# Optimization experiments

Hardware: AMD Instinct MI355X
Metric: run time of the kernel (lower is better)

The kernel has to match this reference:

```python
import jax, jax.numpy as jnp
import numpy as np

N_NODES = 4096
EDGE_PROB = 0.01


def setup_inputs() -> dict:
    key = jax.random.key(0)
    kx, ka, kw = jax.random.split(key, 3)
    x = jax.random.normal(kx, (4, 32, N_NODES, 12), dtype=jnp.float32)
    u = jax.random.uniform(ka, (N_NODES, N_NODES), dtype=jnp.float32)
    adj = (u < EDGE_PROB).astype(jnp.float32)
    adj = jnp.maximum(adj, adj.T)
    weight = jax.random.normal(kw, (3, 32, 32), dtype=jnp.float32) * 0.1
    bias = jnp.zeros((32,), dtype=jnp.float32)
    return {"x": x, "adj": adj, "weight": weight, "bias": bias}


def reference(x, adj, weight, bias):
    # x: [B, c_in, N, T] -> [B, T, N, c_in] as in AdaptiveGraphConv.forward
    B, C, N, T = x.shape
    h = jnp.transpose(x, (0, 3, 2, 1))  # [B, T, N, C]
    # DenseChebConv (K=3): L = I - D^{-1/2} A D^{-1/2}, inf -> 0 for isolated nodes
    d = adj.sum(axis=-1)
    d_inv_sqrt = jnp.where(d > 0, jnp.where(d > 0, d, 1.0) ** -0.5, 0.0)
    norm_adj = d_inv_sqrt[:, None] * adj * d_inv_sqrt[None, :]
    L = jnp.eye(N, dtype=x.dtype) - norm_adj
    Tx0 = h
    Tx1 = jnp.einsum('mn,btnc->btmc', L, h)
    Tx2 = 2.0 * jnp.einsum('mn,btnc->btmc', L, Tx1) - Tx0
    out = (jnp.einsum('btnc,co->btno', Tx0, weight[0])
           + jnp.einsum('btnc,co->btno', Tx1, weight[1])
           + jnp.einsum('btnc,co->btno', Tx2, weight[2])
           + bias)
    # back to [B, c_out, N, T]
    return jnp.transpose(out, (0, 3, 2, 1))
```

## Files before the change

### kernel.cpp

```cpp
#include <hip/hip_runtime.h>

#define NN 4096
#define CC 32
#define TT 12
#define BB 4
#define BT 48
#define NC 1536
#define MAXD 192
#define FW 256
#define NCH 6
#define STP 36
#define SOP 33

typedef float f32x4 __attribute__((ext_vector_type(4)));
typedef short short8 __attribute__((ext_vector_type(8)));

__device__ __forceinline__ float bf2f(unsigned short h) {
  return __uint_as_float(((unsigned int)h) << 16);
}
__device__ __forceinline__ unsigned short f2bf(float f) {
  unsigned int u = __float_as_uint(f);
  return (unsigned short)((u + 0x7FFFu + ((u >> 16) & 1u)) >> 16);
}
__device__ __forceinline__ float blo(unsigned int w) { return __uint_as_float(w << 16); }
__device__ __forceinline__ float bhi(unsigned int w) { return __uint_as_float(w & 0xFFFF0000u); }

__global__ __launch_bounds__(256) void k_build(const float* __restrict__ adj,
                                               uint2* __restrict__ edges,
                                               int* __restrict__ deg, float* __restrict__ dis) {
  __shared__ int cnt;
  int m = blockIdx.x;
  if (threadIdx.x == 0) cnt = 0;
  __syncthreads();
  unsigned int* ecol = (unsigned int*)(edges + m * MAXD);
  const uint4* row = (const uint4*)(adj + (size_t)m * NN);
  for (int i = threadIdx.x; i < NN / 4; i += 256) {
    uint4 v = row[i];
    unsigned int ws[4] = {v.x, v.y, v.z, v.w};
    #pragma unroll
    for (int k = 0; k < 4; ++k) {
      if (ws[k] != 0) {
        int p = atomicAdd(&cnt, 1);
        if (p < MAXD) ecol[p * 2] = (unsigned int)(i * 4 + k);
      }
    }
  }
  __syncthreads();
  if (threadIdx.x == 0) {
    int d = cnt < MAXD ? cnt : MAXD;
    deg[m] = d;
    dis[m] = d > 0 ? (float)(1.0 / sqrt((double)d)) : 0.0f;
  }
}

__global__ __launch_bounds__(192) void k_wt(uint2* __restrict__ edges,
                                            const int* __restrict__ deg,
                                            int* __restrict__ degp,
                                            const float* __restrict__ dis) {
  int m = blockIdx.x;
  int j = threadIdx.x;
  int d = deg[m];
  int dp = (d + 15) & ~15;
  if (j < d) {
    unsigned int* e = (unsigned int*)(edges + m * MAXD + j);
    e[1] = __float_as_uint(dis[e[0]]);
  } else if (j < dp) {
    edges[m * MAXD + j] = make_uint2((unsigned int)m, 0u);
  }
  if (j == 0) degp[m] = dp;
}

__global__ __launch_bounds__(256) void k_trans(const float* __restrict__ x,
                                               unsigned short* __restrict__ H) {
  __shared__ unsigned short sT[192 * STP];
  int b = blockIdx.x >> 8;
  int n0 = (blockIdx.x & 255) * 16;
  int c = threadIdx.x >> 3;
  int l8 = threadIdx.x & 7;
  size_t base = ((size_t)(b * CC + c) * NN + n0) * TT;
  #pragma unroll
  for (int it = 0; it < 6; ++it) {
    int j0 = it * 32 + l8 * 4;
    float4 f = *(const float4*)(x + base + j0);
    sT[(j0 + 0) * STP + c] = f2bf(f.x);
    sT[(j0 + 1) * STP + c] = f2bf(f.y);
    sT[(j0 + 2) * STP + c] = f2bf(f.z);
    sT[(j0 + 3) * STP + c] = f2bf(f.w);
  }
  __syncthreads();
  #pragma unroll
  for (int k = 0; k < 6; ++k) {
    int p = (threadIdx.x >> 3) + 32 * k;
    int nl = p / TT, t = p - nl * TT;
    ushort4 v = *(const ushort4*)&sT[p * STP + l8 * 4];
    size_t off = ((size_t)(n0 + nl) * BT + b * TT + t) * CC + l8 * 4;
    *(ushort4*)(H + off) = v;
  }
}

__global__ __launch_bounds__(256) void k_gather1(const unsigned short* __restrict__ H,
                                                 const uint2* __restrict__ edges,
                                                 const int* __restrict__ degp,
                                                 const float* __restrict__ dis,
                                                 unsigned short* __restrict__ T1) {
  int wid = __builtin_amdgcn_readfirstlane(threadIdx.x >> 6);
  int lane = threadIdx.x & 63;
  int m = blockIdx.x * 4 + wid;
  int d = degp[m];
  float dm = dis[m];
  const uint2* ep = edges + m * MAXD;
  int fo = blockIdx.y * FW + lane * 4;
  const unsigned short* Hf = H + fo;
  float a0 = 0.f, a1 = 0.f, a2 = 0.f, a3 = 0.f;
  #pragma unroll 16
  for (int e = 0; e < d; ++e) {
    uint2 ew = ep[e];
    int cc = (int)ew.x;
    float w = __uint_as_float(ew.y);
    uint2 hv = *(const uint2*)(Hf + cc * NC);
    a0 = fmaf(w, blo(hv.x), a0); a1 = fmaf(w, bhi(hv.x), a1);
    a2 = fmaf(w, blo(hv.y), a2); a3 = fmaf(w, bhi(hv.y), a3);
  }
  uint2 hm = *(const uint2*)(Hf + m * NC);
  ushort4 o;
  o.x = f2bf(blo(hm.x) - dm * a0); o.y = f2bf(bhi(hm.x) - dm * a1);
  o.z = f2bf(blo(hm.y) - dm * a2); o.w = f2bf(bhi(hm.y) - dm * a3);
  *(ushort4*)(T1 + (size_t)m * NC + fo) = o;
}

__global__ __launch_bounds__(256) void k_gather2(const unsigned short* __restrict__ H,
                                                 const unsigned short* __restrict__ T1,
                                                 const uint2* __restrict__ edges,
                                                 const int* __restrict__ degp,
                                                 const float* __restrict__ dis,
                                                 unsigned short* __restrict__ T2) {
  int wid = __builtin_amdgcn_readfirstlane(threadIdx.x >> 6);
  int lane = threadIdx.x & 63;
  int m = blockIdx.x * 4 + wid;
  int d = degp[m];
  float dm = dis[m];
  const uint2* ep = edges + m * MAXD;
  int fo = blockIdx.y * FW + lane * 4;
  const unsigned short* Tf = T1 + fo;
  float a0 = 0.f, a1 = 0.f, a2 = 0.f, a3 = 0.f;
  #pragma unroll 16
  for (int e = 0; e < d; ++e) {
    uint2 ew = ep[e];
    int cc = (int)ew.x;
    float w = __uint_as_float(ew.y);
    uint2 hv = *(const uint2*)(Tf + cc * NC);
    a0 = fmaf(w, blo(hv.x), a0); a1 = fmaf(w, bhi(hv.x), a1);
    a2 = fmaf(w, blo(hv.y), a2); a3 = fmaf(w, bhi(hv.y), a3);
  }
  uint2 tm = *(const uint2*)(Tf + m * NC);
  uint2 hm = *(const uint2*)(H + (size_t)m * NC + fo);
  float td = 2.f * dm;
  ushort4 o;
  o.x = f2bf(2.f * blo(tm.x) - td * a0 - blo(hm.x));
  o.y = f2bf(2.f * bhi(tm.x) - td * a1 - bhi(hm.x));
  o.z = f2bf(2.f * blo(tm.y) - td * a2 - blo(hm.y));
  o.w = f2bf(2.f * bhi(tm.y) - td * a3 - bhi(hm.y));
  *(ushort4*)(T2 + (size_t)m * NC + fo) = o;
}

__global__ __launch_bounds__(256) void k_mix(const unsigned short* __restrict__ H,
                                             const unsigned short* __restrict__ T1,
                                             const unsigned short* __restrict__ T2,
                                             const float* __restrict__ W,
                                             const float* __restrict__ bias,
                                             float* __restrict__ out) {
  __shared__ __align__(16) float sOut[192 * SOP];
  int wid = threadIdx.x >> 6, lane = threadIdx.x & 63;
  int lm = lane & 15, quad = lane >> 4;
  short8 bhf[2][3], blf[2][3];
  float bias0[2];
  for (int h = 0; h < 2; ++h)
    for (int g = 0; g < 3; ++g) {
      short8 vh, vl;
      #pragma unroll
      for (int j = 0; j < 8; ++j) {
        float w = W[(g * CC + quad * 8 + j) * CC + h * 16 + lm];
        unsigned short hi = f2bf(w);
        vh[j] = (short)hi;
        vl[j] = (short)f2bf(w - bf2f(hi));
      }
      bhf[h][g] = vh; blf[h][g] = vl;
    }
  #pragma unroll
  for (int h = 0; h < 2; ++h) bias0[h] = bias[h * 16 + lm];
  int n0 = blockIdx.x * 4;
  #pragma unroll
  for (int tI = 0; tI < 3; ++tI) {
    int r0l = wid * BT + tI * 16;
    size_t abase = ((size_t)(n0 * BT) + r0l + lm) * CC + quad * 8;
    short8 af0 = *(const short8*)(H + abase);
    short8 af1 = *(const short8*)(T1 + abase);
    short8 af2 = *(const short8*)(T2 + abase);
    #pragma unroll
    for (int h = 0; h < 2; ++h) {
      f32x4 acc = {bias0[h], bias0[h], bias0[h], bias0[h]};
      acc = __builtin_amdgcn_mfma_f32_16x16x32_bf16(af0, bhf[h][0], acc, 0, 0, 0);
      acc = __builtin_amdgcn_mfma_f32_16x16x32_bf16(af0, blf[h][0], acc, 0, 0, 0);
      acc = __builtin_amdgcn_mfma_f32_16x16x32_bf16(af1, bhf[h][1], acc, 0, 0, 0);
      acc = __builtin_amdgcn_mfma_f32_16x16x32_bf16(af1, blf[h][1], acc, 0, 0, 0);
      acc = __builtin_amdgcn_mfma_f32_16x16x32_bf16(af2, bhf[h][2], acc, 0, 0, 0);
      acc = __builtin_amdgcn_mfma_f32_16x16x32_bf16(af2, blf[h][2], acc, 0, 0, 0);
      int o = h * 16 + lm;
      #pragma unroll
      for (int reg = 0; reg < 4; ++reg)
        sOut[(r0l + quad * 4 + reg) * SOP + o] = acc[reg];
    }
  }
  __syncthreads();
  #pragma unroll
  for (int j = 0; j < 6; ++j) {
    int idx = j * 256 + threadIdx.x;
    int bo = idx / 12;
    int fq = idx - bo * 12;
    int p0 = fq * 4;
    float v[4];
    #pragma unroll
    for (int k = 0; k < 4; ++k) {
      int p = p0 + k;
      int nl = p / TT, t = p - nl * TT;
      int b = bo >> 5, o = bo & 31;
      v[k] = sOut[(nl * BT + b * TT + t) * SOP + o];
    }
    size_t base = (((size_t)bo * NN) + n0) * TT + p0;
    *(float4*)(out + base) = make_float4(v[0], v[1], v[2], v[3]);
  }
}

extern "C" void kernel_launch(void* const* d_in, const int* in_sizes, int n_in,
                              void* d_out, int out_size, void* d_ws, size_t ws_size,
                              hipStream_t stream) {
  const float* x    = (const float*)d_in[0];
  const float* adj  = (const float*)d_in[1];
  const float* wgt  = (const float*)d_in[2];
  const float* bias = (const float*)d_in[3];
  char* ws = (char*)d_ws;
  float* dis  = (float*)ws;
  int*   deg  = (int*)(ws + 16384);
  int*   degp = (int*)(ws + 32768);
  uint2* edges = (uint2*)(ws + 49152);
  char* p = ws + 49152 + (size_t)NN * MAXD * 8;
  unsigned short* H  = (unsigned short*)p;
  unsigned short* T1 = (unsigned short*)(p + (size_t)NN * NC * 2);
  unsigned short* T2 = (unsigned short*)(p + (size_t)NN * NC * 4);

  k_build<<<NN, 256, 0, stream>>>(adj, edges, deg, dis);
  k_wt<<<NN, 192, 0, stream>>>(edges, deg, degp, dis);
  k_trans<<<1024, 256, 0, stream>>>(x, H);
  k_gather1<<<dim3(NN / 4, NCH), 256, 0, stream>>>(H, edges, degp, dis, T1);
  k_gather2<<<dim3(NN / 4, NCH), 256, 0, stream>>>(H, T1, edges, degp, dis, T2);
  k_mix<<<NN / 4, 256, 0, stream>>>(H, T1, T2, wgt, bias, (float*)d_out);
}
```

Baseline: 274.3 us.

## Fold Chebyshev recurrence into mixed weights and batch wider edge gathers

The two Chebyshev gather kernels become one generic normalized-adjacency gather, G = D^-1/2 A D^-1/2 S, applied twice (G1 from H, G2 from G1). The identity and recurrence terms are folded into the mix weights: W0+W1+W2 for H, -W1-4W2 for G1, and 2W2 for G2. This removes the extra self-row reads and elementwise work from the gathers. The gather loop now issues eight independent 16-byte neighbor loads per step, each thread covering 8 features, with half as many feature chunks, to raise memory-level parallelism. The loop steps eight edges at a time, so it relies on the padded degree and edge list being zero-weight padded to a multiple of 8. Storing the pure aggregates in bf16 also shifts where rounding error enters.

```diff
diff --git a/kernel.cpp b/kernel.cpp
--- a/kernel.cpp
+++ b/kernel.cpp
@@ -7,13 +7,14 @@
 #define BT 48
 #define NC 1536
 #define MAXD 192
-#define FW 256
-#define NCH 6
+#define FW 512
+#define NCH 3
 #define STP 36
 #define SOP 33
 
 typedef float f32x4 __attribute__((ext_vector_type(4)));
 typedef short short8 __attribute__((ext_vector_type(8)));
+typedef unsigned short ushort8 __attribute__((ext_vector_type(8)));
 
 __device__ __forceinline__ float bf2f(unsigned short h) {
   return __uint_as_float(((unsigned int)h) << 16);
@@ -98,74 +99,50 @@
   }
 }
 
-__global__ __launch_bounds__(256) void k_gather1(const unsigned short* __restrict__ H,
-                                                 const uint2* __restrict__ edges,
-                                                 const int* __restrict__ degp,
-                                                 const float* __restrict__ dis,
-                                                 unsigned short* __restrict__ T1) {
+__global__ __launch_bounds__(256) void k_gather(const unsigned short* __restrict__ S,
+                                                const uint2* __restrict__ edges,
+                                                const int* __restrict__ degp,
+                                                const float* __restrict__ dis,
+                                                unsigned short* __restrict__ D) {
   int wid = __builtin_amdgcn_readfirstlane(threadIdx.x >> 6);
   int lane = threadIdx.x & 63;
   int m = blockIdx.x * 4 + wid;
   int d = degp[m];
   float dm = dis[m];
   const uint2* ep = edges + m * MAXD;
-  int fo = blockIdx.y * FW + lane * 4;
-  const unsigned short* Hf = H + fo;
+  int fo = blockIdx.y * FW + lane * 8;
+  const unsigned short* Sf = S + fo;
   float a0 = 0.f, a1 = 0.f, a2 = 0.f, a3 = 0.f;
-  #pragma unroll 16
-  for (int e = 0; e < d; ++e) {
-    uint2 ew = ep[e];
-    int cc = (int)ew.x;
-    float w = __uint_as_float(ew.y);
-    uint2 hv = *(const uint2*)(Hf + cc * NC);
-    a0 = fmaf(w, blo(hv.x), a0); a1 = fmaf(w, bhi(hv.x), a1);
-    a2 = fmaf(w, blo(hv.y), a2); a3 = fmaf(w, bhi(hv.y), a3);
-  }
-  uint2 hm = *(const uint2*)(Hf + m * NC);
-  ushort4 o;
-  o.x = f2bf(blo(hm.x) - dm * a0); o.y = f2bf(bhi(hm.x) - dm * a1);
-  o.z = f2bf(blo(hm.y) - dm * a2); o.w = f2bf(bhi(hm.y) - dm * a3);
-  *(ushort4*)(T1 + (size_t)m * NC + fo) = o;
-}
-
-__global__ __launch_bounds__(256) void k_gather2(const unsigned short* __restrict__ H,
-                                                 const unsigned short* __restrict__ T1,
-                                                 const uint2* __restrict__ edges,
-                                                 const int* __restrict__ degp,
-                                                 const float* __restrict__ dis,
-                                                 unsigned short* __restrict__ T2) {
-  int wid = __builtin_amdgcn_readfirstlane(threadIdx.x >> 6);
-  int lane = threadIdx.x & 63;
-  int m = blockIdx.x * 4 + wid;
-  int d = degp[m];
-  float dm = dis[m];
-  const uint2* ep = edges + m * MAXD;
-  int fo = blockIdx.y * FW + lane * 4;
-  const unsigned short* Tf = T1 + fo;
-  float a0 = 0.f, a1 = 0.f, a2 = 0.f, a3 = 0.f;
-  #pragma unroll 16
-  for (int e = 0; e < d; ++e) {
-    uint2 ew = ep[e];
-    int cc = (int)ew.x;
-    float w = __uint_as_float(ew.y);
-    uint2 hv = *(const uint2*)(Tf + cc * NC);
-    a0 = fmaf(w, blo(hv.x), a0); a1 = fmaf(w, bhi(hv.x), a1);
-    a2 = fmaf(w, blo(hv.y), a2); a3 = fmaf(w, bhi(hv.y), a3);
-  }
-  uint2 tm = *(const uint2*)(Tf + m * NC);
-  uint2 hm = *(const uint2*)(H + (size_t)m * NC + fo);
-  float td = 2.f * dm;
-  ushort4 o;
-  o.x = f2bf(2.f * blo(tm.x) - td * a0 - blo(hm.x));
-  o.y = f2bf(2.f * bhi(tm.x) - td * a1 - bhi(hm.x));
-  o.z = f2bf(2.f * blo(tm.y) - td * a2 - blo(hm.y));
-  o.w = f2bf(2.f * bhi(tm.y) - td * a3 - bhi(hm.y));
-  *(ushort4*)(T2 + (size_t)m * NC + fo) = o;
+  float a4 = 0.f, a5 = 0.f, a6 = 0.f, a7 = 0.f;
+  for (int e = 0; e < d; e += 8) {
+    uint4 hv[8];
+    float w[8];
+    #pragma unroll
+    for (int k = 0; k < 8; ++k) {
+      uint2 ew = ep[e + k];
+      w[k] = __uint_as_float(ew.y);
+      hv[k] = *(const uint4*)(Sf + (int)ew.x * NC);
+    }
+    #pragma unroll
+    for (int k = 0; k < 8; ++k) {
+      float wk = w[k];
+      a0 = fmaf(wk, blo(hv[k].x), a0); a1 = fmaf(wk, bhi(hv[k].x), a1);
+      a2 = fmaf(wk, blo(hv[k].y), a2); a3 = fmaf(wk, bhi(hv[k].y), a3);
+      a4 = fmaf(wk, blo(hv[k].z), a4); a5 = fmaf(wk, bhi(hv[k].z), a5);
+      a6 = fmaf(wk, blo(hv[k].w), a6); a7 = fmaf(wk, bhi(hv[k].w), a7);
+    }
+  }
+  ushort8 o;
+  o[0] = f2bf(dm * a0); o[1] = f2bf(dm * a1);
+  o[2] = f2bf(dm * a2); o[3] = f2bf(dm * a3);
+  o[4] = f2bf(dm * a4); o[5] = f2bf(dm * a5);
+  o[6] = f2bf(dm * a6); o[7] = f2bf(dm * a7);
+  *(ushort8*)(D + (size_t)m * NC + fo) = o;
 }
 
 __global__ __launch_bounds__(256) void k_mix(const unsigned short* __restrict__ H,
-                                             const unsigned short* __restrict__ T1,
-                                             const unsigned short* __restrict__ T2,
+                                             const unsigned short* __restrict__ G1,
+                                             const unsigned short* __restrict__ G2,
                                              const float* __restrict__ W,
                                              const float* __restrict__ bias,
                                              float* __restrict__ out) {
@@ -179,7 +156,13 @@
       short8 vh, vl;
       #pragma unroll
       for (int j = 0; j < 8; ++j) {
-        float w = W[(g * CC + quad * 8 + j) * CC + h * 16 + lm];
+        int r = quad * 8 + j, c = h * 16 + lm;
+        float w0 = W[(0 * CC + r) * CC + c];
+        float w1 = W[(1 * CC + r) * CC + c];
+        float w2 = W[(2 * CC + r) * CC + c];
+        float w = (g == 0) ? (w0 + w1 + w2)
+                 : (g == 1) ? (-w1 - 4.f * w2)
+                            : (2.f * w2);
         unsigned short hi = f2bf(w);
         vh[j] = (short)hi;
         vl[j] = (short)f2bf(w - bf2f(hi));
@@ -194,8 +177,8 @@
     int r0l = wid * BT + tI * 16;
     size_t abase = ((size_t)(n0 * BT) + r0l + lm) * CC + quad * 8;
     short8 af0 = *(const short8*)(H + abase);
-    short8 af1 = *(const short8*)(T1 + abase);
-    short8 af2 = *(const short8*)(T2 + abase);
+    short8 af1 = *(const short8*)(G1 + abase);
+    short8 af2 = *(const short8*)(G2 + abase);
     #pragma unroll
     for (int h = 0; h < 2; ++h) {
       f32x4 acc = {bias0[h], bias0[h], bias0[h], bias0[h]};
@@ -245,13 +228,13 @@
   uint2* edges = (uint2*)(ws + 49152);
   char* p = ws + 49152 + (size_t)NN * MAXD * 8;
   unsigned short* H  = (unsigned short*)p;
-  unsigned short* T1 = (unsigned short*)(p + (size_t)NN * NC * 2);
-  unsigned short* T2 = (unsigned short*)(p + (size_t)NN * NC * 4);
+  unsigned short* G1 = (unsigned short*)(p + (size_t)NN * NC * 2);
+  unsigned short* G2 = (unsigned short*)(p + (size_t)NN * NC * 4);
 
   k_build<<<NN, 256, 0, stream>>>(adj, edges, deg, dis);
   k_wt<<<NN, 192, 0, stream>>>(edges, deg, degp, dis);
   k_trans<<<1024, 256, 0, stream>>>(x, H);
-  k_gather1<<<dim3(NN / 4, NCH), 256, 0, stream>>>(H, edges, degp, dis, T1);
-  k_gather2<<<dim3(NN / 4, NCH), 256, 0, stream>>>(H, T1, edges, degp, dis, T2);
-  k_mix<<<NN / 4, 256, 0, stream>>>(H, T1, T2, wgt, bias, (float*)d_out);
-}
+  k_gather<<<dim3(NN / 4, NCH), 256, 0, stream>>>(H, edges, degp, dis, G1);
+  k_gather<<<dim3(NN / 4, NCH), 256, 0, stream>>>(G1, edges, degp, dis, G2);
+  k_mix<<<NN / 4, 256, 0, stream>>>(H, G1, G2, wgt, bias, (float*)d_out);
+}
```

Result: faster. 241.0 us (-12.1%).
